# Kernel tuning notes

Measured on AMD Instinct MI355X. Metric: run time of the kernel, lower is better.

The kernel has to match this reference:

```python
import jax, jax.numpy as jnp
import numpy as np
import math

B, T, D, M, V = 16, 256, 256, 32, 50257
EPS = 1e-6


def setup_inputs() -> dict:
    key = jax.random.key(0)
    ks = jax.random.split(key, 24)
    s = 0.02
    inp = {
        'hidden_state': jax.random.normal(ks[0], (B, 2, D), jnp.float32),
        'output_sequence': jax.random.randint(ks[1], (B, T), 0, V),
        # embedding table for output tokens
        'emb_out': jax.random.normal(ks[2], (V, D), jnp.float32) * s,
        # decoder_attention (Wq,Wk,Wv are torch Linear weights [out,in], plus biases)
        'Wq1': jax.random.normal(ks[3], (D, D), jnp.float32) * s,
        'bq1': jnp.zeros((D,), jnp.float32),
        'Wk1': jax.random.normal(ks[4], (D, D), jnp.float32) * s,
        'bk1': jnp.zeros((D,), jnp.float32),
        'Wv1': jax.random.normal(ks[5], (D, D), jnp.float32) * s,
        'bv1': jnp.zeros((D,), jnp.float32),
        # decoder_attention_2
        'Wq2': jax.random.normal(ks[6], (D, D), jnp.float32) * s,
        'bq2': jnp.zeros((D,), jnp.float32),
        'Wk2': jax.random.normal(ks[7], (D, D), jnp.float32) * s,
        'bk2': jnp.zeros((D,), jnp.float32),
        'Wv2': jax.random.normal(ks[8], (D, D), jnp.float32) * s,
        'bv2': jnp.zeros((D,), jnp.float32),
        # decoder_mover / decoder_mover_2 weights: nn.Linear(D, M).weight -> [M, D]
        'mover1': jax.random.normal(ks[9], (M, D), jnp.float32) * s,
        'mover2': jax.random.normal(ks[10], (M, D), jnp.float32) * s,
        # norm2
        'gamma': jnp.ones((D,), jnp.float32),
        'beta': jnp.zeros((D,), jnp.float32),
        # vocab logits linear [V, D] + bias
        'Wvoc': jax.random.normal(ks[11], (V, D), jnp.float32) * s,
        'bvoc': jnp.zeros((V,), jnp.float32),
    }
    return inp


def _attn(q, kv, Wq, bq, Wk, bk, Wv, bv):
    # q: [B,1,D], kv: [B,M+1,D]
    Q = q @ Wq.T + bq
    K = kv @ Wk.T + bk
    Vv = kv @ Wv.T + bv
    s = jnp.einsum('bqd,bkd->bqk', Q, K) / jnp.sqrt(jnp.asarray(Q.shape[-1], Q.dtype))
    a = jax.nn.softmax(s, axis=-1)
    return jnp.einsum('bqk,bkd->bqd', a, Vv)


def _layernorm(x, gamma, beta):
    mu = jnp.mean(x, axis=-1, keepdims=True)
    var = jnp.mean((x - mu) ** 2, axis=-1, keepdims=True)
    return (x - mu) * jax.lax.rsqrt(var + EPS) * gamma + beta


def reference(hidden_state, output_sequence, emb_out,
              Wq1, bq1, Wk1, bk1, Wv1, bv1,
              Wq2, bq2, Wk2, bk2, Wv2, bv2,
              mover1, mover2, gamma, beta, Wvoc, bvoc):
    d = emb_out.shape[1]
    # Embeddings: lookup scaled by sqrt(d) (standard simple-transformer embedding)
    x = emb_out[output_sequence] * jnp.sqrt(jnp.asarray(d, jnp.float32))  # [B,T,D]
    z0 = hidden_state[:, 0:1, :]
    z1 = hidden_state[:, 1:2, :]
    b = z0.shape[0]
    mv1 = jnp.broadcast_to(mover1[None], (b, mover1.shape[0], d))  # static per step
    mv2 = jnp.broadcast_to(mover2[None], (b, mover2.shape[0], d))

    def step(carry, xt):
        z0, z1 = carry
        z0 = z0 + xt[:, None, :]
        g = jnp.concatenate([z0, mv1], axis=1)          # [B,M+1,D]
        dg = _attn(g[:, :1], g, Wq1, bq1, Wk1, bk1, Wv1, bv1)
        g2 = jnp.concatenate([z1, mv2], axis=1)
        dg2 = _attn(g2[:, :1], g2, Wq2, bq2, Wk2, bk2, Wv2, bv2)
        z0 = _layernorm(z0 + dg + dg2, gamma, beta)
        return (z0, z0), None

    (z0, z1), _ = jax.lax.scan(step, (z0, z1), jnp.swapaxes(x, 0, 1))
    logits = z0 @ Wvoc.T + bvoc                         # [B,1,V]
    y = jax.nn.log_softmax(logits, axis=-1)
    return jnp.concatenate([z0, z1], axis=1), y
```

## Files before the change

### kernel.cpp

```cpp
#include <hip/hip_runtime.h>

typedef unsigned int u32;
typedef unsigned short u16;

#define DD 256
#define TT 256
#define MM 32
#define NBATCH 16
#define VV 50257

#define WS_FLAG   0
#define WS_KV     16
#define WS_A      32784
#define WS_W12S   163856
#define WS_CB     180240
#define WS_E12    180752
#define WS_CST    180816
#define WS_ZFIN   180832
#define WS_SSUM   184928
#define WS_WPK    184944
#define WS_US     332400
#define WS_SYNC   369264

#if defined(__has_builtin)
#if __has_builtin(__builtin_amdgcn_fdot2)
#define HAS_FDOT2 1
#endif
#endif

typedef _Float16 half2_t __attribute__((ext_vector_type(2)));

__device__ __forceinline__ float bf2f(u16 v){ return __uint_as_float(((u32)v) << 16); }
__device__ __forceinline__ float ldf(const void* p, size_t i, int bf){
  return bf ? bf2f(((const u16*)p)[i]) : ((const float*)p)[i];
}
__device__ __forceinline__ u32 packh2(float a, float b){
  union { half2_t h; u32 u; } x;
  x.h[0] = (_Float16)a; x.h[1] = (_Float16)b;
  return x.u;
}
__device__ __forceinline__ float fdot2(u32 a, u32 b, float c){
  union { u32 u; half2_t h; } ua, ub;
  ua.u = a; ub.u = b;
#ifdef HAS_FDOT2
  return __builtin_amdgcn_fdot2(ua.h, ub.h, c, false);
#else
  return c + (float)ua.h[0]*(float)ub.h[0] + (float)ua.h[1]*(float)ub.h[1];
#endif
}
__device__ __forceinline__ void stv(float* p, float v){
  __hip_atomic_store(p, v, __ATOMIC_RELAXED, __HIP_MEMORY_SCOPE_SYSTEM);
}
__device__ __forceinline__ float ldv(const float* p){
  return __hip_atomic_load(p, __ATOMIC_RELAXED, __HIP_MEMORY_SCOPE_SYSTEM);
}

__global__ void k_init(const u32* gam, u32* flag, float* Ssum, u32* sync){
  if (threadIdx.x == 0) *flag = (gam[0] == 0x3F800000u) ? 0u : 1u;
  if (threadIdx.x < 16) Ssum[threadIdx.x] = 0.f;
  for (int i = threadIdx.x; i < 512; i += 256) sync[i] = 0u;
}

__global__ __launch_bounds__(256) void k_prep1(
  const void* Wk1, const void* bk1, const void* Wv1, const void* bv1,
  const void* Wk2, const void* bk2, const void* Wv2, const void* bv2,
  const void* m1, const void* m2, float* KV, const u32* flagp)
{
  const int bf = (int)*flagp;
  int mat = blockIdx.x >> 5, j = blockIdx.x & 31, d = threadIdx.x;
  const void *W, *bias, *mv;
  if (mat == 0){ W = Wk1; bias = bk1; mv = m1; }
  else if (mat == 1){ W = Wv1; bias = bv1; mv = m1; }
  else if (mat == 2){ W = Wk2; bias = bk2; mv = m2; }
  else { W = Wv2; bias = bv2; mv = m2; }
  float acc = ldf(bias, d, bf);
  for (int e = 0; e < DD; ++e) acc += ldf(W, d*DD + e, bf) * ldf(mv, j*DD + e, bf);
  KV[mat*8192 + j*DD + d] = acc;
}

__global__ __launch_bounds__(256) void k_prep2(
  const void* Wq1, const void* Wk1, const void* bq1, const void* bk1,
  const void* Wq2, const void* Wk2, const void* bq2, const void* bk2,
  const float* KV, float* A, float* W12s, float* cb, float* e12, float* cst,
  const u32* flagp)
{
  const int bf = (int)*flagp;
  int blk = blockIdx.x, tid = threadIdx.x;
  if (blk < 512){
    int mat = blk >> 8, i = blk & 255;
    const void* Wq = mat ? Wq2 : Wq1;
    const void* Wk = mat ? Wk2 : Wk1;
    float acc = 0.f;
    for (int e = 0; e < DD; ++e) acc += ldf(Wq, e*DD + i, bf) * ldf(Wk, e*DD + tid, bf);
    A[mat*65536 + i*DD + tid] = acc;
  } else if (blk < 576){
    int idx = blk - 512, mat = idx >> 5, j = idx & 31;
    const void* Wq = mat ? Wq2 : Wq1;
    const float* K = KV + mat*16384;
    float acc = 0.f;
    for (int e = 0; e < DD; ++e) acc += ldf(Wq, e*DD + tid, bf) * K[j*DD + e];
    W12s[mat*8192 + j*DD + tid] = acc;
  } else if (blk < 578){
    int mat = blk - 576;
    const void* Wq = mat ? Wq2 : Wq1;
    const void* Wk = mat ? Wk2 : Wk1;
    const void* bq = mat ? bq2 : bq1;
    const void* bk = mat ? bk2 : bk1;
    float acc = 0.f;
    for (int e = 0; e < DD; ++e)
      acc += ldf(Wk, e*DD + tid, bf) * ldf(bq, e, bf) + ldf(Wq, e*DD + tid, bf) * ldf(bk, e, bf);
    cb[mat*DD + tid] = acc;
  } else {
    if (tid < 32){
      float acc = 0.f;
      for (int d = 0; d < DD; ++d) acc += ldf(bq1, d, bf) * KV[tid*DD + d];
      e12[tid] = acc;
    } else if (tid < 64){
      int j = tid - 32; float acc = 0.f;
      for (int d = 0; d < DD; ++d) acc += ldf(bq2, d, bf) * KV[16384 + j*DD + d];
      e12[32 + j] = acc;
    } else if (tid == 64){
      float acc = 0.f;
      for (int d = 0; d < DD; ++d) acc += ldf(bq1, d, bf) * ldf(bk1, d, bf);
      cst[0] = acc;
    } else if (tid == 65){
      float acc = 0.f;
      for (int d = 0; d < DD; ++d) acc += ldf(bq2, d, bf) * ldf(bk2, d, bf);
      cst[1] = acc;
    }
  }
}

__global__ __launch_bounds__(256) void k_pack(
  const float* __restrict__ A, const float* __restrict__ W12s,
  const float* __restrict__ cb, const void* __restrict__ Wv1,
  const void* __restrict__ Wv2, u32* __restrict__ Wpk, const u32* flagp)
{
  const int bf = (int)*flagp;
  int idx = blockIdx.x*256 + threadIdx.x;
  float v0 = 0.f, v1 = 0.f;
  if (idx < 131072){
    int p = idx >> 15;
    int r2 = idx & 32767;
    int e2g = r2 >> 10;
    int t = (r2 >> 2) & 255;
    int q = r2 & 3;
    int c = e2g*8 + q*2;
    if (p == 0){ v0 = A[t*DD + c]; v1 = A[t*DD + c + 1]; }
    else if (p == 1){ v0 = ldf(Wv1, t*DD + c, bf); v1 = ldf(Wv1, t*DD + c + 1, bf); }
    else if (p == 2){ v0 = A[65536 + t*DD + c]; v1 = A[65536 + t*DD + c + 1]; }
    else { v0 = ldf(Wv2, t*DD + c, bf); v1 = ldf(Wv2, t*DD + c + 1, bf); }
  } else {
    int rem = idx - 131072;
    int t = rem >> 7;
    int e2g = (rem >> 2) & 31;
    int q = rem & 3;
    int c = e2g*8 + q*2;
    if (t < 32){ v0 = W12s[t*DD + c]; v1 = W12s[t*DD + c + 1]; }
    else if (t < 64){ v0 = W12s[8192 + (t-32)*DD + c]; v1 = W12s[8192 + (t-32)*DD + c + 1]; }
    else if (t == 64){ v0 = cb[c]; v1 = cb[c + 1]; }
    else if (t == 65){ v0 = cb[DD + c]; v1 = cb[DD + c + 1]; }
  }
  Wpk[idx] = packh2(v0, v1);
}

__global__ __launch_bounds__(256) void k_seq(
    const void* __restrict__ hid, const int* __restrict__ seq,
    const void* __restrict__ emb,
    const u32* __restrict__ Wpk, const float* __restrict__ V1g,
    const float* __restrict__ V2g, const float* __restrict__ e1g,
    const float* __restrict__ e2g_, const float* __restrict__ cst,
    const void* __restrict__ bv1, const void* __restrict__ bv2,
    const void* __restrict__ gam, const void* __restrict__ bet,
    float* __restrict__ zfin, float* __restrict__ out0,
    const u32* __restrict__ flagp, float* __restrict__ usg,
    u32* __restrict__ syncg)
{
  __shared__ float z0s[DD], z1s[DD];
  __shared__ __align__(16) u32 zp0[128], zp1[128];
  __shared__ u32 V1h[MM*DD/2], V2h[MM*DD/2];
  __shared__ float a1s[33], a2s[33];
  __shared__ float red[16];
  __shared__ float gs[DD], bs[DD], bv1s[DD], bv2s[DD];
  __shared__ float e1s[MM], e2s[MM];
  __shared__ int toks[TT];

  const int tid = threadIdx.x;
  const int wg = blockIdx.x;
  const int b = wg >> 2;
  const int g = wg & 3;
  const int lane = tid & 63;
  const int wv = tid >> 6;
  const int bf = (int)*flagp;

  float* us0 = usg + b*2304;
  float* us1 = us0 + 1152;
  u32* flag = syncg + b*32;

  for (int r = tid; r < MM*DD/2; r += 256){
    V1h[r] = packh2(V1g[2*r], V1g[2*r + 1]);
    V2h[r] = packh2(V2g[2*r], V2g[2*r + 1]);
  }
  for (int r = tid; r < TT; r += 256) toks[r] = seq[b*TT + r];
  gs[tid] = ldf(gam, tid, bf); bs[tid] = ldf(bet, tid, bf);
  bv1s[tid] = ldf(bv1, tid, bf); bv2s[tid] = ldf(bv2, tid, bf);
  if (tid < MM){ e1s[tid] = e1g[tid]; e2s[tid] = e2g_[tid]; }
  const float c1 = cst[0], c2 = cst[1];
  __syncthreads();
  z1s[tid] = ldf(hid, b*2*DD + DD + tid, bf);
  z0s[tid] = ldf(hid, b*2*DD + tid, bf) + ldf(emb, (size_t)toks[0]*DD + tid, bf) * 16.0f;
  __syncthreads();

  const uint4* Wp = (const uint4*)Wpk;
  const uint4* wpMain = Wp + g*8192 + tid;
  const int p4row = g*32 + (tid >> 3);
  const uint4* wpP4 = Wp + 32768 + p4row*32 + (tid & 7);
  const bool p4z1 = (p4row >= 32 && p4row < 64) || (p4row == 65);

  for (int t = 0; t < TT; ++t){
    float* usw = (t & 1) ? us1 : us0;
    float xnext = 0.f;
    if (t + 1 < TT) xnext = ldf(emb, (size_t)toks[t+1]*DD + tid, bf) * 16.0f;

    if (tid < 128) zp0[tid] = packh2(z0s[2*tid], z0s[2*tid+1]);
    else { int i = tid - 128; zp1[i] = packh2(z1s[2*i], z1s[2*i+1]); }
    __syncthreads();

    {
      const uint4* zp4 = (const uint4*)((g < 2) ? zp0 : zp1);
      float a0 = 0.f, a1 = 0.f, a2 = 0.f, a3 = 0.f;
      #pragma unroll 8
      for (int k = 0; k < 32; ++k){
        uint4 w = wpMain[k*256];
        uint4 z = zp4[k];
        a0 = fdot2(w.x, z.x, a0);
        a1 = fdot2(w.y, z.y, a1);
        a2 = fdot2(w.z, z.z, a2);
        a3 = fdot2(w.w, z.w, a3);
      }
      stv(&usw[g*256 + tid], (a0 + a1) + (a2 + a3));
    }
    {
      const uint4* zq = (const uint4*)(p4z1 ? zp1 : zp0);
      float a0 = 0.f, a1 = 0.f, a2 = 0.f, a3 = 0.f;
      #pragma unroll
      for (int j = 0; j < 4; ++j){
        uint4 w = wpP4[j*8];
        uint4 z = zq[(tid & 7) + 8*j];
        a0 = fdot2(w.x, z.x, a0);
        a1 = fdot2(w.y, z.y, a1);
        a2 = fdot2(w.z, z.z, a2);
        a3 = fdot2(w.w, z.w, a3);
      }
      float s = (a0 + a1) + (a2 + a3);
      s += __shfl_down(s, 4, 64);
      s += __shfl_down(s, 2, 64);
      s += __shfl_down(s, 1, 64);
      if ((tid & 7) == 0) stv(&usw[1024 + p4row], s);
    }

    __threadfence_block();
    __syncthreads();
    if (tid == 0)
      __hip_atomic_store(&flag[g*8], (u32)(t+1), __ATOMIC_RELAXED, __HIP_MEMORY_SCOPE_SYSTEM);
    if (tid < 4){
      while (__hip_atomic_load(&flag[tid*8], __ATOMIC_RELAXED, __HIP_MEMORY_SCOPE_SYSTEM) < (u32)(t+1)) {}
    }
    __syncthreads();

    const float* usr = usw;
    float u0  = ldv(&usr[tid]);
    float uv1 = ldv(&usr[256 + tid]);
    float u2  = ldv(&usr[512 + tid]);
    float uv2 = ldv(&usr[768 + tid]);

    float p1 = z0s[tid] * u0;
    float p2 = z1s[tid] * u2;
    #pragma unroll
    for (int off = 32; off; off >>= 1){
      p1 += __shfl_down(p1, off, 64);
      p2 += __shfl_down(p2, off, 64);
    }
    if (lane == 0){ red[wv] = p1; red[4 + wv] = p2; }
    __syncthreads();
    if (tid == 0) a1s[0] = (red[0]+red[1]+red[2]+red[3] + ldv(&usr[1088]) + c1) * 0.0625f;
    if (tid == 1) a2s[0] = (red[4]+red[5]+red[6]+red[7] + ldv(&usr[1089]) + c2) * 0.0625f;
    if (tid >= 64 && tid < 96)  a1s[tid - 63] = (ldv(&usr[1024 + (tid-64)]) + e1s[tid-64]) * 0.0625f;
    if (tid >= 96 && tid < 128) a2s[tid - 95] = (ldv(&usr[1056 + (tid-96)]) + e2s[tid-96]) * 0.0625f;
    __syncthreads();

    if (tid < 128){
      float* sm = (tid < 64) ? a1s : a2s;
      float v = (lane < 33) ? sm[lane] : -1e30f;
      float mx = v;
      #pragma unroll
      for (int off = 32; off; off >>= 1) mx = fmaxf(mx, __shfl_xor(mx, off, 64));
      float e = (lane < 33) ? expf(v - mx) : 0.f;
      float s = e;
      #pragma unroll
      for (int off = 32; off; off >>= 1) s += __shfl_xor(s, off, 64);
      if (lane < 33) sm[lane] = e / s;
    }
    __syncthreads();

    float hv1 = uv1 + bv1s[tid];
    float hv2 = uv2 + bv2s[tid];
    float dg = a1s[0] * hv1;
    float dh = a2s[0] * hv2;
    int half_idx = tid >> 1;
    #pragma unroll
    for (int j = 1; j <= 32; ++j){
      union { u32 u; half2_t h; } pv1, pv2;
      pv1.u = V1h[((j-1) << 7) + half_idx];
      pv2.u = V2h[((j-1) << 7) + half_idx];
      float e1v = (tid & 1) ? (float)pv1.h[1] : (float)pv1.h[0];
      float e2v = (tid & 1) ? (float)pv2.h[1] : (float)pv2.h[0];
      dg += a1s[j] * e1v;
      dh += a2s[j] * e2v;
    }
    float y = z0s[tid] + dg + dh;
    float sy = y, syy = y * y;
    #pragma unroll
    for (int off = 32; off; off >>= 1){
      sy += __shfl_down(sy, off, 64);
      syy += __shfl_down(syy, off, 64);
    }
    if (lane == 0){ red[8 + wv] = sy; red[12 + wv] = syy; }
    __syncthreads();
    float Sy = red[8] + red[9] + red[10] + red[11];
    float Syy = red[12] + red[13] + red[14] + red[15];
    float mu = Sy * (1.f/DD);
    float var = Syy * (1.f/DD) - mu*mu;
    float zi = (y - mu) * rsqrtf(var + 1e-6f) * gs[tid] + bs[tid];
    if (t == TT - 1){
      if (g == 0){
        zfin[b*DD + tid] = zi;
        out0[b*2*DD + tid] = zi;
        out0[b*2*DD + DD + tid] = zi;
      }
    } else {
      z1s[tid] = zi;
      z0s[tid] = zi + xnext;
    }
    __syncthreads();
  }
}

__global__ __launch_bounds__(256) void k_logits(
    const float* __restrict__ zfin, const void* __restrict__ Wvoc,
    const void* __restrict__ bvoc, float* __restrict__ Ssum,
    float* __restrict__ out1, const u32* __restrict__ flagp)
{
  __shared__ float zfs[NBATCH][DD];
  const int tid = threadIdx.x;
  const int bf = (int)*flagp;
  for (int r = tid; r < NBATCH*DD; r += 256) zfs[r >> 8][r & 255] = zfin[r];
  __syncthreads();

  const int v = blockIdx.x*256 + tid;
  float acc[NBATCH];
  const bool ok = (v < VV);
  float bias = ok ? ldf(bvoc, v, bf) : 0.f;
  #pragma unroll
  for (int b = 0; b < NBATCH; ++b) acc[b] = bias;

  if (ok){
    if (bf){
      const uint4* wr = ((const uint4*)Wvoc) + (size_t)v*32;
      for (int gg = 0; gg < 32; ++gg){
        uint4 u = wr[gg];
        float w0 = __uint_as_float(u.x << 16), w1 = __uint_as_float(u.x & 0xffff0000u);
        float w2 = __uint_as_float(u.y << 16), w3 = __uint_as_float(u.y & 0xffff0000u);
        float w4 = __uint_as_float(u.z << 16), w5 = __uint_as_float(u.z & 0xffff0000u);
        float w6 = __uint_as_float(u.w << 16), w7 = __uint_as_float(u.w & 0xffff0000u);
        const int c = gg*8;
        #pragma unroll
        for (int b = 0; b < NBATCH; ++b){
          const float* zc = &zfs[b][c];
          acc[b] += w0*zc[0] + w1*zc[1] + w2*zc[2] + w3*zc[3]
                  + w4*zc[4] + w5*zc[5] + w6*zc[6] + w7*zc[7];
        }
      }
    } else {
      const float4* wr = ((const float4*)Wvoc) + (size_t)v*64;
      for (int gg = 0; gg < 64; ++gg){
        float4 u = wr[gg];
        const int c = gg*4;
        #pragma unroll
        for (int b = 0; b < NBATCH; ++b){
          const float* zc = &zfs[b][c];
          acc[b] += u.x*zc[0] + u.y*zc[1] + u.z*zc[2] + u.w*zc[3];
        }
      }
    }
    #pragma unroll
    for (int b = 0; b < NBATCH; ++b) out1[(size_t)b*VV + v] = acc[b];
  }

  #pragma unroll
  for (int b = 0; b < NBATCH; ++b){
    float p = ok ? expf(acc[b]) : 0.f;
    #pragma unroll
    for (int off = 32; off; off >>= 1) p += __shfl_down(p, off, 64);
    if ((tid & 63) == 0) atomicAdd(&Ssum[b], p);
  }
}

__global__ __launch_bounds__(256) void k_final(
    const float* __restrict__ Ssum, float* __restrict__ out1)
{
  const int v = blockIdx.x*256 + threadIdx.x;
  const int b = blockIdx.y;
  if (v < VV){
    float ls = logf(Ssum[b]);
    size_t i = (size_t)b*VV + v;
    out1[i] = out1[i] - ls;
  }
}

extern "C" void kernel_launch(void* const* d_in, const int* in_sizes, int n_in,
                              void* d_out, int out_size, void* d_ws, size_t ws_size,
                              hipStream_t stream)
{
  (void)in_sizes; (void)n_in; (void)out_size; (void)ws_size;
  const void* hid  = d_in[0];
  const int*  seq  = (const int*)d_in[1];
  const void* emb  = d_in[2];
  const void* Wq1  = d_in[3];
  const void* bq1  = d_in[4];
  const void* Wk1  = d_in[5];
  const void* bk1  = d_in[6];
  const void* Wv1  = d_in[7];
  const void* bv1  = d_in[8];
  const void* Wq2  = d_in[9];
  const void* bq2  = d_in[10];
  const void* Wk2  = d_in[11];
  const void* bk2  = d_in[12];
  const void* Wv2  = d_in[13];
  const void* bv2  = d_in[14];
  const void* m1   = d_in[15];
  const void* m2   = d_in[16];
  const void* gam  = d_in[17];
  const void* bet  = d_in[18];
  const void* Wvoc = d_in[19];
  const void* bvoc = d_in[20];

  float* wsf    = (float*)d_ws;
  u32*   flag   = (u32*)(wsf + WS_FLAG);
  float* KV     = wsf + WS_KV;
  float* A      = wsf + WS_A;
  float* W12s   = wsf + WS_W12S;
  float* cb     = wsf + WS_CB;
  float* e12    = wsf + WS_E12;
  float* cst    = wsf + WS_CST;
  float* zfin   = wsf + WS_ZFIN;
  float* Ssum   = wsf + WS_SSUM;
  u32*   Wpk    = (u32*)(wsf + WS_WPK);
  float* usg    = wsf + WS_US;
  u32*   syncg  = (u32*)(wsf + WS_SYNC);

  float* out0 = (float*)d_out;
  float* out1 = out0 + NBATCH*2*DD;

  k_init<<<1, 256, 0, stream>>>((const u32*)gam, flag, Ssum, syncg);
  k_prep1<<<128, 256, 0, stream>>>(Wk1,bk1,Wv1,bv1,Wk2,bk2,Wv2,bv2,m1,m2,KV,flag);
  k_prep2<<<579, 256, 0, stream>>>(Wq1,Wk1,bq1,bk1,Wq2,Wk2,bq2,bk2,KV,A,W12s,cb,e12,cst,flag);
  k_pack<<<576, 256, 0, stream>>>(A,W12s,cb,Wv1,Wv2,Wpk,flag);
  k_seq<<<NBATCH*4, 256, 0, stream>>>(hid, seq, emb, Wpk, KV+8192, KV+24576,
                                      e12, e12+32, cst, bv1, bv2, gam, bet, zfin, out0,
                                      flag, usg, syncg);
  k_logits<<<197, 256, 0, stream>>>(zfin, Wvoc, bvoc, Ssum, out1, flag);
  k_final<<<dim3(197, NBATCH), 256, 0, stream>>>(Ssum, out1);
}
```

Measured before the change: 1.855 ms.

## Replace per-step flag barrier with tagged data words for cross-block sync

The per-timestep inter-workgroup handshake (block barrier, flag store, spin on four flags, second barrier) is replaced by embedding a parity tag in the low mantissa bit of each exchanged float. Each thread spins directly on the values it needs until all carry the current tag. The exchange buffer is pre-initialised with the opposite tag in k_init. This removes two __syncthreads and a flag round trip per step on the serial 256-step critical path, at the cost of losing one mantissa bit and relying on the ordering of relaxed atomics.

```diff
diff --git a/kernel.cpp b/kernel.cpp
--- a/kernel.cpp
+++ b/kernel.cpp
@@ -48,17 +48,25 @@
   return c + (float)ua.h[0]*(float)ub.h[0] + (float)ua.h[1]*(float)ub.h[1];
 #endif
 }
-__device__ __forceinline__ void stv(float* p, float v){
+__device__ __forceinline__ u32 ldu(const u32* p){
+  return __hip_atomic_load(p, __ATOMIC_RELAXED, __HIP_MEMORY_SCOPE_SYSTEM);
+}
+__device__ __forceinline__ void stu(u32* p, u32 v){
   __hip_atomic_store(p, v, __ATOMIC_RELAXED, __HIP_MEMORY_SCOPE_SYSTEM);
 }
-__device__ __forceinline__ float ldv(const float* p){
-  return __hip_atomic_load(p, __ATOMIC_RELAXED, __HIP_MEMORY_SCOPE_SYSTEM);
-}
-
-__global__ void k_init(const u32* gam, u32* flag, float* Ssum, u32* sync){
-  if (threadIdx.x == 0) *flag = (gam[0] == 0x3F800000u) ? 0u : 1u;
-  if (threadIdx.x < 16) Ssum[threadIdx.x] = 0.f;
-  for (int i = threadIdx.x; i < 512; i += 256) sync[i] = 0u;
+__device__ __forceinline__ void stv_tag(float* p, float v, u32 tag){
+  stu((u32*)p, (__float_as_uint(v) & ~1u) | tag);
+}
+
+__global__ __launch_bounds__(256) void k_init(const u32* gam, u32* flag,
+                                              float* Ssum, u32* sync, u32* usg){
+  const int gtid = blockIdx.x*256 + threadIdx.x;
+  if (blockIdx.x == 0){
+    if (threadIdx.x == 0) *flag = (gam[0] == 0x3F800000u) ? 0u : 1u;
+    if (threadIdx.x < 16) Ssum[threadIdx.x] = 0.f;
+    for (int i = threadIdx.x; i < 512; i += 256) sync[i] = 0u;
+  }
+  for (int i = gtid; i < NBATCH*2304; i += 8*256) stu(&usg[i], 1u);
 }
 
 __global__ __launch_bounds__(256) void k_prep1(
@@ -176,6 +184,7 @@
     const u32* __restrict__ flagp, float* __restrict__ usg,
     u32* __restrict__ syncg)
 {
+  (void)syncg;
   __shared__ float z0s[DD], z1s[DD];
   __shared__ __align__(16) u32 zp0[128], zp1[128];
   __shared__ u32 V1h[MM*DD/2], V2h[MM*DD/2];
@@ -195,7 +204,6 @@
 
   float* us0 = usg + b*2304;
   float* us1 = us0 + 1152;
-  u32* flag = syncg + b*32;
 
   for (int r = tid; r < MM*DD/2; r += 256){
     V1h[r] = packh2(V1g[2*r], V1g[2*r + 1]);
@@ -217,8 +225,14 @@
   const uint4* wpP4 = Wp + 32768 + p4row*32 + (tid & 7);
   const bool p4z1 = (p4row >= 32 && p4row < 64) || (p4row == 65);
 
+  int xi;
+  if (tid < 2) xi = 1088 + tid;
+  else if (tid >= 64 && tid < 128) xi = 1024 + (tid - 64);
+  else xi = tid;
+
   for (int t = 0; t < TT; ++t){
     float* usw = (t & 1) ? us1 : us0;
+    const u32 tg = (u32)((t >> 1) & 1);
     float xnext = 0.f;
     if (t + 1 < TT) xnext = ldf(emb, (size_t)toks[t+1]*DD + tid, bf) * 16.0f;
 
@@ -238,7 +252,7 @@
         a2 = fdot2(w.z, z.z, a2);
         a3 = fdot2(w.w, z.w, a3);
       }
-      stv(&usw[g*256 + tid], (a0 + a1) + (a2 + a3));
+      stv_tag(&usw[g*256 + tid], (a0 + a1) + (a2 + a3), tg);
     }
     {
       const uint4* zq = (const uint4*)(p4z1 ? zp1 : zp0);
@@ -256,23 +270,27 @@
       s += __shfl_down(s, 4, 64);
       s += __shfl_down(s, 2, 64);
       s += __shfl_down(s, 1, 64);
-      if ((tid & 7) == 0) stv(&usw[1024 + p4row], s);
-    }
-
-    __threadfence_block();
-    __syncthreads();
-    if (tid == 0)
-      __hip_atomic_store(&flag[g*8], (u32)(t+1), __ATOMIC_RELAXED, __HIP_MEMORY_SCOPE_SYSTEM);
-    if (tid < 4){
-      while (__hip_atomic_load(&flag[tid*8], __ATOMIC_RELAXED, __HIP_MEMORY_SCOPE_SYSTEM) < (u32)(t+1)) {}
-    }
-    __syncthreads();
-
-    const float* usr = usw;
-    float u0  = ldv(&usr[tid]);
-    float uv1 = ldv(&usr[256 + tid]);
-    float u2  = ldv(&usr[512 + tid]);
-    float uv2 = ldv(&usr[768 + tid]);
+      if ((tid & 7) == 0) stv_tag(&usw[1024 + p4row], s, tg);
+    }
+
+    u32 b0, b1, b2, b3, bx;
+    {
+      const u32* up = (const u32*)usw;
+      for (;;){
+        b0 = ldu(up + tid);
+        b1 = ldu(up + 256 + tid);
+        b2 = ldu(up + 512 + tid);
+        b3 = ldu(up + 768 + tid);
+        bx = ldu(up + xi);
+        if ((((b0 ^ tg) | (b1 ^ tg) | (b2 ^ tg) | (b3 ^ tg) | (bx ^ tg)) & 1u) == 0u)
+          break;
+      }
+    }
+    float u0  = __uint_as_float(b0);
+    float uv1 = __uint_as_float(b1);
+    float u2  = __uint_as_float(b2);
+    float uv2 = __uint_as_float(b3);
+    float xf  = __uint_as_float(bx);
 
     float p1 = z0s[tid] * u0;
     float p2 = z1s[tid] * u2;
@@ -283,10 +301,10 @@
     }
     if (lane == 0){ red[wv] = p1; red[4 + wv] = p2; }
     __syncthreads();
-    if (tid == 0) a1s[0] = (red[0]+red[1]+red[2]+red[3] + ldv(&usr[1088]) + c1) * 0.0625f;
-    if (tid == 1) a2s[0] = (red[4]+red[5]+red[6]+red[7] + ldv(&usr[1089]) + c2) * 0.0625f;
-    if (tid >= 64 && tid < 96)  a1s[tid - 63] = (ldv(&usr[1024 + (tid-64)]) + e1s[tid-64]) * 0.0625f;
-    if (tid >= 96 && tid < 128) a2s[tid - 95] = (ldv(&usr[1056 + (tid-96)]) + e2s[tid-96]) * 0.0625f;
+    if (tid == 0) a1s[0] = (red[0]+red[1]+red[2]+red[3] + xf + c1) * 0.0625f;
+    if (tid == 1) a2s[0] = (red[4]+red[5]+red[6]+red[7] + xf + c2) * 0.0625f;
+    if (tid >= 64 && tid < 96)  a1s[tid - 63] = (xf + e1s[tid-64]) * 0.0625f;
+    if (tid >= 96 && tid < 128) a2s[tid - 95] = (xf + e2s[tid-96]) * 0.0625f;
     __syncthreads();
 
     if (tid < 128){
@@ -462,7 +480,7 @@
   float* out0 = (float*)d_out;
   float* out1 = out0 + NBATCH*2*DD;
 
-  k_init<<<1, 256, 0, stream>>>((const u32*)gam, flag, Ssum, syncg);
+  k_init<<<8, 256, 0, stream>>>((const u32*)gam, flag, Ssum, syncg, (u32*)usg);
   k_prep1<<<128, 256, 0, stream>>>(Wk1,bk1,Wv1,bv1,Wk2,bk2,Wv2,bv2,m1,m2,KV,flag);
   k_prep2<<<579, 256, 0, stream>>>(Wq1,Wk1,bq1,bk1,Wq2,Wk2,bq2,bk2,KV,A,W12s,cb,e12,cst,flag);
   k_pack<<<576, 256, 0, stream>>>(A,W12s,cb,Wv1,Wv2,Wpk,flag);
```

Result: faster. 1.788 ms (-3.6%).
